# Performance work log

Measured on AMD Instinct MI355X. Metric: run time of the kernel, lower is better.

## Reference

```python
import jax, jax.numpy as jnp
import numpy as np

BATCH = 8192
MAX_PIECES = 32
NNZ = BATCH * MAX_PIECES
FT_OUT = 512
N_FEATURES = 768


def setup_inputs() -> dict:
    key = jax.random.key(0)
    ks = jax.random.split(key, 8)
    # COO indices: row 0 = batch index (each position contributes MAX_PIECES features),
    # row 1 = feature index in [0, 768)
    batch_ids = jnp.repeat(jnp.arange(BATCH, dtype=jnp.int64), MAX_PIECES)
    stm_feat = jax.random.randint(ks[0], (NNZ,), 0, N_FEATURES, dtype=jnp.int64)
    nstm_feat = jax.random.randint(ks[1], (NNZ,), 0, N_FEATURES, dtype=jnp.int64)
    stm_indices = jnp.stack([batch_ids, stm_feat])   # [2, nnz]
    nstm_indices = jnp.stack([batch_ids, nstm_feat])  # [2, nnz]
    values = jnp.ones((NNZ,), dtype=jnp.float32)      # binary features
    # Linear(768, FT_OUT): store weight transposed as [768, FT_OUT]
    ft_w = jax.random.normal(ks[2], (N_FEATURES, FT_OUT), dtype=jnp.float32) * (1.0 / np.sqrt(N_FEATURES))
    ft_b = jax.random.normal(ks[3], (FT_OUT,), dtype=jnp.float32) * 0.01
    # Linear(2*FT_OUT, 1): stored as [2*FT_OUT, 1]
    out_w = jax.random.normal(ks[4], (2 * FT_OUT, 1), dtype=jnp.float32) * (1.0 / np.sqrt(2 * FT_OUT))
    out_b = jax.random.normal(ks[5], (1,), dtype=jnp.float32) * 0.01
    return {
        "stm_indices": stm_indices,
        "nstm_indices": nstm_indices,
        "values": values,
        "ft_w": ft_w,
        "ft_b": ft_b,
        "out_w": out_w,
        "out_b": out_b,
        "batch_size": BATCH,
    }


def reference(stm_indices, nstm_indices, values, ft_w, ft_b, out_w, out_b, batch_size):
    def feature_transform(indices):
        # sparse @ W^T + b  ==  gather rows of W^T by feature id, scale by value,
        # segment-sum into batch rows. rows: [nnz, FT_OUT]
        rows = ft_w[indices[1]] * values[:, None]
        acc = jax.ops.segment_sum(rows, indices[0], num_segments=batch_size)
        return acc + ft_b

    stm_ft = feature_transform(stm_indices)    # [B, FT_OUT]
    nstm_ft = feature_transform(nstm_indices)  # [B, FT_OUT]
    hidden = jnp.clip(jnp.concatenate([stm_ft, nstm_ft], axis=1), 0.0, 1.0)
    return jax.nn.sigmoid(hidden @ out_w + out_b)  # [B, 1]
```

## Files before the change

### kernel.cpp

```cpp
#include <hip/hip_runtime.h>
#include <math.h>

#define MAX_PIECES 32
#define FT_OUT 512
#define NFEAT 768
#define QSCALE 512.0f
#define INV_QSCALE (1.0f / 512.0f)

typedef unsigned int u32x4 __attribute__((ext_vector_type(4)));

__global__ __launch_bounds__(256) void cvt_i8(
    const float* __restrict__ ft_w, unsigned int* __restrict__ qtab, int n)
{
    const int i = (blockIdx.x * 256 + threadIdx.x) * 4;
    if (i >= n) return;
    const float4 f = *(const float4*)(ft_w + i);
    const float vf[4] = {f.x, f.y, f.z, f.w};
    unsigned int packed = 0;
    #pragma unroll
    for (int j = 0; j < 4; ++j) {
        float q = rintf(vf[j] * QSCALE);
        q = fminf(fmaxf(q, -127.f), 127.f);
        packed |= ((unsigned int)(int)(q + 128.f) & 0xffu) << (8 * j);
    }
    qtab[i >> 2] = packed;
}

__global__ __launch_bounds__(256) void nnue_fwd(
    const int*   __restrict__ stm_idx,
    const int*   __restrict__ nstm_idx,
    const float* __restrict__ values,
    const unsigned char* __restrict__ qtab,
    const float* __restrict__ ft_b,
    const float* __restrict__ out_w,
    const float* __restrict__ out_b,
    float*       __restrict__ out,
    int nnz)
{
    const int t    = threadIdx.x;
    const int g    = t >> 6;
    const int lane = t & 63;
    const int half = lane >> 5;
    const int l31  = lane & 31;
    const int side = g & 1;
    const int row  = blockIdx.x * 2 + (g >> 1);

    __shared__ float s_red[4];

    const int* __restrict__ src = side ? nstm_idx : stm_idx;
    const int meta   = row * MAX_PIECES + l31;
    const int myidx  = src[nnz + meta];
    const int myvali = __float_as_int(values[meta]);

    float acc[16];
    #pragma unroll
    for (int j = 0; j < 16; ++j) acc[j] = 0.f;
    float vsum = 0.f;

    const unsigned char* __restrict__ qbase = qtab + (l31 << 4);

    #pragma unroll
    for (int i = 0; i < 16; ++i) {
        const int   p = 2 * i + half;
        const int   f = __shfl(myidx, p, 64);
        const float v = __int_as_float(__shfl(myvali, p, 64));
        vsum += v;
        const u32x4 u = __builtin_nontemporal_load(
            (const u32x4*)(qbase + ((long)f << 9)));
        #pragma unroll
        for (int k = 0; k < 4; ++k) {
            const unsigned int w = u[k];
            acc[4 * k + 0] = fmaf((float)( w        & 0xffu), v, acc[4 * k + 0]);
            acc[4 * k + 1] = fmaf((float)((w >>  8) & 0xffu), v, acc[4 * k + 1]);
            acc[4 * k + 2] = fmaf((float)((w >> 16) & 0xffu), v, acc[4 * k + 2]);
            acc[4 * k + 3] = fmaf((float)( w >> 24         ), v, acc[4 * k + 3]);
        }
    }

    #pragma unroll
    for (int j = 0; j < 16; ++j) acc[j] += __shfl_xor(acc[j], 32, 64);
    vsum += __shfl_xor(vsum, 32, 64);
    const float qoff = 128.f * vsum;

    const int colb = l31 * 16;
    float pacc = 0.f;
    #pragma unroll
    for (int q = 0; q < 4; ++q) {
        const float4 bb = *(const float4*)(ft_b + colb + 4 * q);
        const float4 ww = *(const float4*)(out_w + side * FT_OUT + colb + 4 * q);
        const float bv[4] = {bb.x, bb.y, bb.z, bb.w};
        const float wv[4] = {ww.x, ww.y, ww.z, ww.w};
        #pragma unroll
        for (int j = 0; j < 4; ++j) {
            const float h = fminf(fmaxf(
                fmaf(acc[4 * q + j] - qoff, INV_QSCALE, bv[j]), 0.f), 1.f);
            pacc = fmaf(h, wv[j], pacc);
        }
    }

    #pragma unroll
    for (int off = 1; off < 64; off <<= 1)
        pacc += __shfl_xor(pacc, off, 64);
    if (lane == 0) s_red[g] = 0.5f * pacc;
    __syncthreads();

    if (t < 2) {
        const float s = s_red[2 * t] + s_red[2 * t + 1] + out_b[0];
        out[blockIdx.x * 2 + t] = 1.f / (1.f + expf(-s));
    }
}

extern "C" void kernel_launch(void* const* d_in, const int* in_sizes, int n_in,
                              void* d_out, int out_size, void* d_ws, size_t ws_size,
                              hipStream_t stream) {
    const int*   stm_idx  = (const int*)d_in[0];
    const int*   nstm_idx = (const int*)d_in[1];
    const float* values   = (const float*)d_in[2];
    const float* ft_w     = (const float*)d_in[3];
    const float* ft_b     = (const float*)d_in[4];
    const float* out_w    = (const float*)d_in[5];
    const float* out_b    = (const float*)d_in[6];
    float*       out      = (float*)d_out;

    const int nnz = in_sizes[0] / 2;
    const int B   = out_size;
    const int nw  = NFEAT * FT_OUT;

    unsigned int* qtab = (unsigned int*)d_ws;

    cvt_i8<<<(nw / 4 + 255) / 256, 256, 0, stream>>>(ft_w, qtab, nw);
    nnue_fwd<<<B / 2, 256, 0, stream>>>(stm_idx, nstm_idx, values,
                                        (const unsigned char*)qtab,
                                        ft_b, out_w, out_b, out, nnz);
}
```

Before: 91.76 us.

## Stage quantized weight slices in LDS and split output columns across blocks

Each block now quantizes a 128-column slice of the feature-transform weights into LDS (96 KB of int8) and gathers rows from shared memory instead of global memory, processing 128 batch rows per block. Index/value metadata is packed into 32-bit words (feature id plus fp16 value) in LDS. Partial dot products per slice are combined with global atomicAdd into the output, followed by a separate sigmoid kernel and a memset. This removes the separate quantization pass and repeated global gathers, but re-quantizes the weights in every block. It also adds atomics, two extra launches, and LDS-limited occupancy.

```diff
diff --git a/kernel.cpp b/kernel.cpp
--- a/kernel.cpp
+++ b/kernel.cpp
@@ -1,113 +1,129 @@
 #include <hip/hip_runtime.h>
+#include <hip/hip_fp16.h>
 #include <math.h>
 
 #define MAX_PIECES 32
 #define FT_OUT 512
 #define NFEAT 768
+#define SLICE 128
+#define NSLICE 4
+#define ROWS_PER_BLOCK 128
+#define THREADS 1024
 #define QSCALE 512.0f
 #define INV_QSCALE (1.0f / 512.0f)
 
-typedef unsigned int u32x4 __attribute__((ext_vector_type(4)));
-
-__global__ __launch_bounds__(256) void cvt_i8(
-    const float* __restrict__ ft_w, unsigned int* __restrict__ qtab, int n)
-{
-    const int i = (blockIdx.x * 256 + threadIdx.x) * 4;
-    if (i >= n) return;
-    const float4 f = *(const float4*)(ft_w + i);
-    const float vf[4] = {f.x, f.y, f.z, f.w};
-    unsigned int packed = 0;
-    #pragma unroll
-    for (int j = 0; j < 4; ++j) {
-        float q = rintf(vf[j] * QSCALE);
-        q = fminf(fmaxf(q, -127.f), 127.f);
-        packed |= ((unsigned int)(int)(q + 128.f) & 0xffu) << (8 * j);
-    }
-    qtab[i >> 2] = packed;
-}
-
-__global__ __launch_bounds__(256) void nnue_fwd(
+__global__ __launch_bounds__(THREADS, 4) void nnue_gather(
     const int*   __restrict__ stm_idx,
     const int*   __restrict__ nstm_idx,
     const float* __restrict__ values,
-    const unsigned char* __restrict__ qtab,
+    const float* __restrict__ ft_w,
     const float* __restrict__ ft_b,
     const float* __restrict__ out_w,
-    const float* __restrict__ out_b,
-    float*       __restrict__ out,
+    float*       __restrict__ acc_out,
     int nnz)
 {
+    const int s    = blockIdx.x & (NSLICE - 1);
+    const int grp  = blockIdx.x >> 2;
     const int t    = threadIdx.x;
-    const int g    = t >> 6;
     const int lane = t & 63;
+    const int w    = t >> 6;
     const int half = lane >> 5;
     const int l31  = lane & 31;
-    const int side = g & 1;
-    const int row  = blockIdx.x * 2 + (g >> 1);
 
-    __shared__ float s_red[4];
-
-    const int* __restrict__ src = side ? nstm_idx : stm_idx;
-    const int meta   = row * MAX_PIECES + l31;
-    const int myidx  = src[nnz + meta];
-    const int myvali = __float_as_int(values[meta]);
-
-    float acc[16];
-    #pragma unroll
-    for (int j = 0; j < 16; ++j) acc[j] = 0.f;
-    float vsum = 0.f;
-
-    const unsigned char* __restrict__ qbase = qtab + (l31 << 4);
+    __shared__ unsigned char s_w[NFEAT * SLICE];
+    __shared__ unsigned int  s_meta[ROWS_PER_BLOCK * 2 * MAX_PIECES];
+    __shared__ float s_bias[SLICE];
+    __shared__ float s_hw[2 * SLICE];
 
     #pragma unroll
-    for (int i = 0; i < 16; ++i) {
-        const int   p = 2 * i + half;
-        const int   f = __shfl(myidx, p, 64);
-        const float v = __int_as_float(__shfl(myvali, p, 64));
-        vsum += v;
-        const u32x4 u = __builtin_nontemporal_load(
-            (const u32x4*)(qbase + ((long)f << 9)));
+    for (int k = 0; k < (NFEAT * SLICE / 4) / THREADS; ++k) {
+        const int id = k * THREADS + t;
+        const int r  = id >> 5;
+        const int c4 = id & 31;
+        const float4 f = ((const float4*)(ft_w + r * FT_OUT + s * SLICE))[c4];
+        const float vf[4] = {f.x, f.y, f.z, f.w};
+        unsigned int packed = 0;
         #pragma unroll
-        for (int k = 0; k < 4; ++k) {
-            const unsigned int w = u[k];
-            acc[4 * k + 0] = fmaf((float)( w        & 0xffu), v, acc[4 * k + 0]);
-            acc[4 * k + 1] = fmaf((float)((w >>  8) & 0xffu), v, acc[4 * k + 1]);
-            acc[4 * k + 2] = fmaf((float)((w >> 16) & 0xffu), v, acc[4 * k + 2]);
-            acc[4 * k + 3] = fmaf((float)( w >> 24         ), v, acc[4 * k + 3]);
+        for (int j = 0; j < 4; ++j) {
+            float q = rintf(vf[j] * QSCALE);
+            q = fminf(fmaxf(q, -127.f), 127.f);
+            packed |= ((unsigned int)(int)(q + 128.f) & 0xffu) << (8 * j);
         }
+        ((unsigned int*)s_w)[r * 32 + c4] = packed;
     }
 
     #pragma unroll
-    for (int j = 0; j < 16; ++j) acc[j] += __shfl_xor(acc[j], 32, 64);
-    vsum += __shfl_xor(vsum, 32, 64);
-    const float qoff = 128.f * vsum;
-
-    const int colb = l31 * 16;
-    float pacc = 0.f;
-    #pragma unroll
-    for (int q = 0; q < 4; ++q) {
-        const float4 bb = *(const float4*)(ft_b + colb + 4 * q);
-        const float4 ww = *(const float4*)(out_w + side * FT_OUT + colb + 4 * q);
-        const float bv[4] = {bb.x, bb.y, bb.z, bb.w};
-        const float wv[4] = {ww.x, ww.y, ww.z, ww.w};
-        #pragma unroll
-        for (int j = 0; j < 4; ++j) {
-            const float h = fminf(fmaxf(
-                fmaf(acc[4 * q + j] - qoff, INV_QSCALE, bv[j]), 0.f), 1.f);
-            pacc = fmaf(h, wv[j], pacc);
-        }
+    for (int k = 0; k < (ROWS_PER_BLOCK * 2 * MAX_PIECES) / THREADS; ++k) {
+        const int e    = k * THREADS + t;
+        const int row  = e >> 6;
+        const int side = (e >> 5) & 1;
+        const int p    = e & 31;
+        const int gi   = (grp * ROWS_PER_BLOCK + row) * MAX_PIECES + p;
+        const int feat = (side ? nstm_idx : stm_idx)[nnz + gi];
+        const float v  = values[gi];
+        s_meta[e] = ((unsigned int)feat << 16) |
+                    (unsigned int)__half_as_ushort(__float2half(v));
     }
 
-    #pragma unroll
-    for (int off = 1; off < 64; off <<= 1)
-        pacc += __shfl_xor(pacc, off, 64);
-    if (lane == 0) s_red[g] = 0.5f * pacc;
+    if (t < SLICE) {
+        s_bias[t] = ft_b[s * SLICE + t];
+    } else if (t < 3 * SLICE) {
+        const int side = (t - SLICE) >> 7, c = (t - SLICE) & (SLICE - 1);
+        s_hw[side * SLICE + c] = out_w[side * FT_OUT + s * SLICE + c];
+    }
     __syncthreads();
 
-    if (t < 2) {
-        const float s = s_red[2 * t] + s_red[2 * t + 1] + out_b[0];
-        out[blockIdx.x * 2 + t] = 1.f / (1.f + expf(-s));
+    const int laneoff = l31 * 4;
+
+    for (int r = 0; r < 8; ++r) {
+        const int rowl = r * 16 + w;
+        const unsigned int* mp = s_meta + rowl * 64 + half * 32;
+
+        float a0 = 0.f, a1 = 0.f, a2 = 0.f, a3 = 0.f, vsum = 0.f;
+
+        #pragma unroll
+        for (int q = 0; q < 8; ++q) {
+            const uint4 m = *(const uint4*)(mp + q * 4);
+            const unsigned int mm[4] = {m.x, m.y, m.z, m.w};
+            #pragma unroll
+            for (int j = 0; j < 4; ++j) {
+                const unsigned int feat = mm[j] >> 16;
+                const float v = __half2float(
+                    __ushort_as_half((unsigned short)(mm[j] & 0xffffu)));
+                vsum += v;
+                const unsigned int u =
+                    *(const unsigned int*)(s_w + feat * SLICE + laneoff);
+                a0 = fmaf((float)( u         & 0xffu), v, a0);
+                a1 = fmaf((float)((u >>  8)  & 0xffu), v, a1);
+                a2 = fmaf((float)((u >> 16)  & 0xffu), v, a2);
+                a3 = fmaf((float)( u >> 24          ), v, a3);
+            }
+        }
+
+        const float qoff = 128.f * vsum;
+        const float4 bb = *(const float4*)(s_bias + laneoff);
+        const float4 hw = *(const float4*)(s_hw + half * SLICE + laneoff);
+        float p;
+        p =      fminf(fmaxf(fmaf(a0 - qoff, INV_QSCALE, bb.x), 0.f), 1.f) * hw.x;
+        p = fmaf(fminf(fmaxf(fmaf(a1 - qoff, INV_QSCALE, bb.y), 0.f), 1.f), hw.y, p);
+        p = fmaf(fminf(fmaxf(fmaf(a2 - qoff, INV_QSCALE, bb.z), 0.f), 1.f), hw.z, p);
+        p = fmaf(fminf(fmaxf(fmaf(a3 - qoff, INV_QSCALE, bb.w), 0.f), 1.f), hw.w, p);
+
+        p += __shfl_xor(p, 1, 64);
+        p += __shfl_xor(p, 2, 64);
+        p += __shfl_xor(p, 4, 64);
+        p += __shfl_xor(p, 8, 64);
+        p += __shfl_xor(p, 16, 64);
+        if (l31 == 0)
+            atomicAdd(acc_out + grp * ROWS_PER_BLOCK + rowl, p);
     }
+}
+
+__global__ __launch_bounds__(256) void nnue_head(
+    float* __restrict__ acc, const float* __restrict__ out_b, int B)
+{
+    const int i = blockIdx.x * 256 + threadIdx.x;
+    if (i < B) acc[i] = 1.f / (1.f + expf(-(acc[i] + out_b[0])));
 }
 
 extern "C" void kernel_launch(void* const* d_in, const int* in_sizes, int n_in,
@@ -124,12 +140,9 @@
 
     const int nnz = in_sizes[0] / 2;
     const int B   = out_size;
-    const int nw  = NFEAT * FT_OUT;
 
-    unsigned int* qtab = (unsigned int*)d_ws;
-
-    cvt_i8<<<(nw / 4 + 255) / 256, 256, 0, stream>>>(ft_w, qtab, nw);
-    nnue_fwd<<<B / 2, 256, 0, stream>>>(stm_idx, nstm_idx, values,
-                                        (const unsigned char*)qtab,
-                                        ft_b, out_w, out_b, out, nnz);
+    hipMemsetAsync(out, 0, B * sizeof(float), stream);
+    nnue_gather<<<NSLICE * (B / ROWS_PER_BLOCK), THREADS, 0, stream>>>(
+        stm_idx, nstm_idx, values, ft_w, ft_b, out_w, out, nnz);
+    nnue_head<<<(B + 255) / 256, 256, 0, stream>>>(out, out_b, B);
 }
```

Result: slower. 102.3 us (+11.4%).
